# Optimization experiments

Measured on AMD Instinct MI355X. Metric: run time of the kernel, lower is better.

The kernel has to match this reference:

```python
import jax, jax.numpy as jnp
from jax import lax
import numpy as np

B, N, K = 8, 4096, 64          # clouds, points per cloud, max neighbors
N1, N2 = N // 2, N // 8        # fps ratio 0.5, then 0.25
R1, R2 = 0.2, 0.4              # ball-query radii


def setup_inputs() -> dict:
    key = jax.random.key(0)
    ks = jax.random.split(key, 7)
    def w(k, i, o):
        return jax.random.normal(k, (i, o), jnp.float32) / np.sqrt(i).astype(np.float32)
    return {
        "pos": jax.random.uniform(ks[0], (B, N, 3), jnp.float32),
        "w1a": w(ks[1], 3, 64),    "b1a": jnp.zeros(64, jnp.float32),
        "w1b": w(ks[2], 64, 64),   "b1b": jnp.zeros(64, jnp.float32),
        "w2a": w(ks[3], 67, 128),  "b2a": jnp.zeros(128, jnp.float32),
        "w2b": w(ks[4], 128, 128), "b2b": jnp.zeros(128, jnp.float32),
        "w3a": w(ks[5], 131, 256), "b3a": jnp.zeros(256, jnp.float32),
        "w3b": w(ks[6], 256, 1024),"b3b": jnp.zeros(1024, jnp.float32),
    }


def fps(pos, n_samples):
    # farthest point sampling, deterministic start at index 0. pos: [n, 3]
    d0 = jnp.sum((pos - pos[0]) ** 2, axis=-1)
    def step(mind, _):
        nxt = jnp.argmax(mind)
        d = jnp.sum((pos - pos[nxt]) ** 2, axis=-1)
        return jnp.minimum(mind, d), nxt
    _, idxs = lax.scan(step, d0, None, length=n_samples - 1)
    return jnp.concatenate([jnp.zeros((1,), idxs.dtype), idxs])


def ball_query(centers, pts, r):
    # up to K neighbors within radius r (nearest-first); centers are a subset of pts
    d2 = jnp.sum((centers[:, None, :] - pts[None, :, :]) ** 2, axis=-1)  # [M, n]
    neg = jnp.where(d2 <= r * r, -d2, -jnp.inf)
    vals, nbr = lax.top_k(neg, K)
    return nbr, vals > -jnp.inf  # [M, K] indices, validity mask


def mlp(x, w1, b1, w2, b2, relu_last):
    h = jax.nn.relu(x @ w1 + b1) @ w2 + b2
    return jax.nn.relu(h) if relu_last else h


def masked_max(h, mask):
    # max over neighbor axis; every center has itself as a valid neighbor
    return jnp.max(jnp.where(mask[..., None], h, -jnp.inf), axis=1)


def reference(pos, w1a, b1a, w1b, b1b, w2a, b2a, w2b, b2b, w3a, b3a, w3b, b3b):
    def single(p):  # p: [N, 3]
        # SA1: x is None -> per-edge input is relative position only
        idx1 = fps(p, N1)
        c1 = p[idx1]                                   # [N1, 3]
        nbr1, m1 = ball_query(c1, p, R1)               # [N1, K]
        rel1 = p[nbr1] - c1[:, None, :]                # [N1, K, 3]
        x1 = masked_max(mlp(rel1, w1a, b1a, w1b, b1b, True), m1)   # [N1, 64]
        # SA2: per-edge input is [x_j, pos_j - pos_i]
        idx2 = fps(c1, N2)
        c2 = c1[idx2]                                  # [N2, 3]
        nbr2, m2 = ball_query(c2, c1, R2)              # [N2, K]
        feat2 = jnp.concatenate([x1[nbr2], c1[nbr2] - c2[:, None, :]], axis=-1)  # [N2,K,67]
        x2 = masked_max(mlp(feat2, w2a, b2a, w2b, b2b, True), m2)  # [N2, 128]
        # Global SA: MLP on [x, pos] then global max pool
        g = mlp(jnp.concatenate([x2, c2], axis=-1), w3a, b3a, w3b, b3b, False)   # [N2,1024]
        return jnp.max(g, axis=0)                      # [1024]
    return jax.vmap(single)(pos)                       # [B, 1024]
```

## Files before the change

### kernel.cpp

```cpp
#include <hip/hip_runtime.h>
#include <cstdint>
#include <cstddef>


static constexpr int Bc = 8;
static constexpr int Np = 4096;
static constexpr int Kn = 64;
static constexpr int M1 = 2048;
static constexpr int M2 = 512;
static constexpr int LDX = 132;

#define DEVINL __device__ __forceinline__

DEVINL float d2_exact(float ax, float ay, float az, float bx, float by, float bz) {
    float dx = __fsub_rn(ax, bx);
    float dy = __fsub_rn(ay, by);
    float dz = __fsub_rn(az, bz);
    float xx = __fmul_rn(dx, dx);
    float yy = __fmul_rn(dy, dy);
    float zz = __fmul_rn(dz, dz);
    return __fadd_rn(__fadd_rn(xx, yy), zz);
}

template <int CTRL, int RM, int BM>
DEVINL unsigned long long dpp_max_step(unsigned long long k) {
    unsigned lo = (unsigned)k, hi = (unsigned)(k >> 32);
    unsigned slo = (unsigned)__builtin_amdgcn_update_dpp(0, (int)lo, CTRL, RM, BM, true);
    unsigned shi = (unsigned)__builtin_amdgcn_update_dpp(0, (int)hi, CTRL, RM, BM, true);
    unsigned long long s = ((unsigned long long)shi << 32) | (unsigned long long)slo;
    return s > k ? s : k;
}

DEVINL unsigned long long wave_max_u64_dpp(unsigned long long k) {
    k = dpp_max_step<0x111, 0xf, 0xf>(k);
    k = dpp_max_step<0x112, 0xf, 0xf>(k);
    k = dpp_max_step<0x114, 0xf, 0xf>(k);
    k = dpp_max_step<0x118, 0xf, 0xf>(k);
    k = dpp_max_step<0x142, 0xa, 0xf>(k);
    k = dpp_max_step<0x143, 0xc, 0xf>(k);
    return k;
}

DEVINL unsigned mort3(unsigned v) {
    return (v & 1u) | ((v & 2u) << 2) | ((v & 4u) << 4);
}

DEVINL unsigned cell_of(float x, float y, float z) {
    int ix = (int)(x * 8.0f); ix = ix < 0 ? 0 : (ix > 7 ? 7 : ix);
    int iy = (int)(y * 8.0f); iy = iy < 0 ? 0 : (iy > 7 ? 7 : iy);
    int iz = (int)(z * 8.0f); iz = iz < 0 ? 0 : (iz > 7 ? 7 : iz);
    return mort3((unsigned)ix) | (mort3((unsigned)iy) << 1) | (mort3((unsigned)iz) << 2);
}

DEVINL unsigned* scan512(unsigned* h0, unsigned* h1, int t) {
    unsigned* src = h0; unsigned* dst = h1;
    for (int d = 1; d < 512; d <<= 1) {
        unsigned v = src[t];
        if (t >= d) v += src[t - d];
        dst[t] = v;
        __syncthreads();
        unsigned* tmp = src; src = dst; dst = tmp;
    }
    return src;
}

__global__ __launch_bounds__(512)
void fps2x_kernel(const float* __restrict__ pos, float* __restrict__ c1,
                  float* __restrict__ c2, float* __restrict__ X) {
    constexpr int NT = 512;
    __shared__ float scx[Np], scy[Np], scz[Np];
    __shared__ unsigned spk[Np];
    __shared__ float s2c[M1 * 3];
    __shared__ unsigned h0[512], h1[512];
    __shared__ unsigned long long slots[3];
    const int b = blockIdx.x;
    const int t = threadIdx.x;
    const int lane = t & 63;

    {
        constexpr int PT = Np / NT;
        const float* base = pos + (size_t)b * Np * 3;
        float gx[PT], gy[PT], gz[PT];
        unsigned gc[PT];
        #pragma unroll
        for (int j = 0; j < PT; ++j) {
            int p = j * NT + t;
            gx[j] = base[p * 3 + 0];
            gy[j] = base[p * 3 + 1];
            gz[j] = base[p * 3 + 2];
            gc[j] = cell_of(gx[j], gy[j], gz[j]);
        }
        float x0 = base[0], y0 = base[1], z0 = base[2];
        h0[t] = 0;
        if (t == 0) { slots[0] = 0; slots[1] = 0; slots[2] = 0; }
        __syncthreads();
        #pragma unroll
        for (int j = 0; j < PT; ++j) atomicAdd(&h0[gc[j]], 1u);
        __syncthreads();
        unsigned cnt = h0[t];
        unsigned* inc = scan512(h0, h1, t);
        inc[t] -= cnt;
        __syncthreads();
        #pragma unroll
        for (int j = 0; j < PT; ++j) {
            unsigned p = atomicAdd(&inc[gc[j]], 1u);
            scx[p] = gx[j]; scy[p] = gy[j]; scz[p] = gz[j];
            spk[p] = ((0xFFFu - (unsigned)(j * NT + t)) << 12) | p;
        }
        __syncthreads();

        float px[PT], py[PT], pz[PT], mind[PT];
        unsigned oi[PT];
        #pragma unroll
        for (int j = 0; j < PT; ++j) {
            int p = t * PT + j;
            px[j] = scx[p]; py[j] = scy[p]; pz[j] = scz[p];
            oi[j] = spk[p];
        }
        float lox = px[0], hix = px[0], loy = py[0], hiy = py[0], loz = pz[0], hiz = pz[0];
        #pragma unroll
        for (int j = 1; j < PT; ++j) {
            lox = fminf(lox, px[j]); hix = fmaxf(hix, px[j]);
            loy = fminf(loy, py[j]); hiy = fmaxf(hiy, py[j]);
            loz = fminf(loz, pz[j]); hiz = fmaxf(hiz, pz[j]);
        }

        unsigned long long ck = 0;
        #pragma unroll
        for (int j = 0; j < PT; ++j) {
            float d = d2_exact(px[j], py[j], pz[j], x0, y0, z0);
            mind[j] = d;
            unsigned long long kj =
                ((unsigned long long)__float_as_uint(d) << 24) | (unsigned long long)oi[j];
            if (kj > ck) ck = kj;
        }
        float bmax = __uint_as_float((unsigned)(ck >> 24));
        unsigned long long wkey = wave_max_u64_dpp(ck);
        if (lane == 63) atomicMax(&slots[1], wkey);
        if (t == 0) {
            c1[((size_t)b * M1) * 3 + 0] = x0;
            c1[((size_t)b * M1) * 3 + 1] = y0;
            c1[((size_t)b * M1) * 3 + 2] = z0;
            s2c[0] = x0; s2c[1] = y0; s2c[2] = z0;
        }
        int rd = 1, wr = 2, rs = 0;
        for (int s = 1; s < M1; ++s) {
            __syncthreads();
            unsigned long long km = slots[rd];
            if (t == 0) slots[rs] = 0;
            unsigned spos = (unsigned)km & 0xFFFu;
            float cx = scx[spos], cy = scy[spos], cz = scz[spos];
            if (t == 0) {
                c1[((size_t)b * M1 + s) * 3 + 0] = cx;
                c1[((size_t)b * M1 + s) * 3 + 1] = cy;
                c1[((size_t)b * M1 + s) * 3 + 2] = cz;
                s2c[s * 3 + 0] = cx; s2c[s * 3 + 1] = cy; s2c[s * 3 + 2] = cz;
            }
            float dxv = fmaxf(fmaxf(lox - cx, cx - hix), 0.0f);
            float dyv = fmaxf(fmaxf(loy - cy, cy - hiy), 0.0f);
            float dzv = fmaxf(fmaxf(loz - cz, cz - hiz), 0.0f);
            float L = dxv * dxv + dyv * dyv + dzv * dzv;
            bool fire = (L * 0.999f <= bmax);
            if (fire) {
                unsigned long long nck = 0;
                #pragma unroll
                for (int j = 0; j < PT; ++j) {
                    float d = d2_exact(px[j], py[j], pz[j], cx, cy, cz);
                    float m = fminf(mind[j], d);
                    mind[j] = m;
                    unsigned long long kj =
                        ((unsigned long long)__float_as_uint(m) << 24) | (unsigned long long)oi[j];
                    if (kj > nck) nck = kj;
                }
                ck = nck;
                bmax = __uint_as_float((unsigned)(ck >> 24));
            }
            if (__ballot(fire) != 0ull) wkey = wave_max_u64_dpp(ck);
            if (lane == 63) atomicMax(&slots[wr], wkey);
            int nrd = wr; wr = rs; rs = rd; rd = nrd;
        }
    }
    __syncthreads();

    {
        constexpr int PT = M1 / NT;
        float gx[PT], gy[PT], gz[PT];
        unsigned gc[PT];
        #pragma unroll
        for (int j = 0; j < PT; ++j) {
            int p = j * NT + t;
            gx[j] = s2c[p * 3 + 0];
            gy[j] = s2c[p * 3 + 1];
            gz[j] = s2c[p * 3 + 2];
            gc[j] = cell_of(gx[j], gy[j], gz[j]);
        }
        float x0 = s2c[0], y0 = s2c[1], z0 = s2c[2];
        h0[t] = 0;
        if (t == 0) { slots[0] = 0; slots[1] = 0; slots[2] = 0; }
        __syncthreads();
        #pragma unroll
        for (int j = 0; j < PT; ++j) atomicAdd(&h0[gc[j]], 1u);
        __syncthreads();
        unsigned cnt = h0[t];
        unsigned* inc = scan512(h0, h1, t);
        inc[t] -= cnt;
        __syncthreads();
        #pragma unroll
        for (int j = 0; j < PT; ++j) {
            unsigned p = atomicAdd(&inc[gc[j]], 1u);
            scx[p] = gx[j]; scy[p] = gy[j]; scz[p] = gz[j];
            spk[p] = ((0xFFFu - (unsigned)(j * NT + t)) << 12) | p;
        }
        __syncthreads();

        float px[PT], py[PT], pz[PT], mind[PT];
        unsigned oi[PT];
        #pragma unroll
        for (int j = 0; j < PT; ++j) {
            int p = t * PT + j;
            px[j] = scx[p]; py[j] = scy[p]; pz[j] = scz[p];
            oi[j] = spk[p];
        }
        float lox = px[0], hix = px[0], loy = py[0], hiy = py[0], loz = pz[0], hiz = pz[0];
        #pragma unroll
        for (int j = 1; j < PT; ++j) {
            lox = fminf(lox, px[j]); hix = fmaxf(hix, px[j]);
            loy = fminf(loy, py[j]); hiy = fmaxf(hiy, py[j]);
            loz = fminf(loz, pz[j]); hiz = fmaxf(hiz, pz[j]);
        }

        unsigned long long ck = 0;
        #pragma unroll
        for (int j = 0; j < PT; ++j) {
            float d = d2_exact(px[j], py[j], pz[j], x0, y0, z0);
            mind[j] = d;
            unsigned long long kj =
                ((unsigned long long)__float_as_uint(d) << 24) | (unsigned long long)oi[j];
            if (kj > ck) ck = kj;
        }
        float bmax = __uint_as_float((unsigned)(ck >> 24));
        unsigned long long wkey = wave_max_u64_dpp(ck);
        if (lane == 63) atomicMax(&slots[1], wkey);
        if (t == 0) {
            c2[((size_t)b * M2) * 3 + 0] = x0;
            c2[((size_t)b * M2) * 3 + 1] = y0;
            c2[((size_t)b * M2) * 3 + 2] = z0;
            float* xr = X + (size_t)(b * M2) * LDX;
            xr[128] = x0; xr[129] = y0; xr[130] = z0;
        }
        int rd = 1, wr = 2, rs = 0;
        for (int s = 1; s < M2; ++s) {
            __syncthreads();
            unsigned long long km = slots[rd];
            if (t == 0) slots[rs] = 0;
            unsigned spos = (unsigned)km & 0xFFFu;
            float cx = scx[spos], cy = scy[spos], cz = scz[spos];
            if (t == 0) {
                c2[((size_t)b * M2 + s) * 3 + 0] = cx;
                c2[((size_t)b * M2 + s) * 3 + 1] = cy;
                c2[((size_t)b * M2 + s) * 3 + 2] = cz;
                float* xr = X + (size_t)(b * M2 + s) * LDX;
                xr[128] = cx; xr[129] = cy; xr[130] = cz;
            }
            float dxv = fmaxf(fmaxf(lox - cx, cx - hix), 0.0f);
            float dyv = fmaxf(fmaxf(loy - cy, cy - hiy), 0.0f);
            float dzv = fmaxf(fmaxf(loz - cz, cz - hiz), 0.0f);
            float L = dxv * dxv + dyv * dyv + dzv * dzv;
            bool fire = (L * 0.999f <= bmax);
            if (fire) {
                unsigned long long nck = 0;
                #pragma unroll
                for (int j = 0; j < PT; ++j) {
                    float d = d2_exact(px[j], py[j], pz[j], cx, cy, cz);
                    float m = fminf(mind[j], d);
                    mind[j] = m;
                    unsigned long long kj =
                        ((unsigned long long)__float_as_uint(m) << 24) | (unsigned long long)oi[j];
                    if (kj > nck) nck = kj;
                }
                ck = nck;
                bmax = __uint_as_float((unsigned)(ck >> 24));
            }
            if (__ballot(fire) != 0ull) wkey = wave_max_u64_dpp(ck);
            if (lane == 63) atomicMax(&slots[wr], wkey);
            int nrd = wr; wr = rs; rs = rd; rd = nrd;
        }
    }
}

template <int NPT>
__global__ __launch_bounds__(256)
void bq_kernel(const float* __restrict__ pts, const float* __restrict__ ctr,
               int mshift, float r2, int* __restrict__ nbr) {
    constexpr int CH = NPT / 64;
    constexpr int CAP = 1024;
    __shared__ uint2 cbuf[4][CAP];
    const int lane = threadIdx.x & 63;
    const int wl = threadIdx.x >> 6;
    int w = __builtin_amdgcn_readfirstlane((int)(blockIdx.x * 4 + wl));
    const int b = w >> mshift;
    const float* pb = pts + (size_t)b * NPT * 3;
    const float* cp = ctr + (size_t)w * 3;
    float cx = cp[0], cy = cp[1], cz = cp[2];
    const unsigned r2b = __float_as_uint(r2);

    unsigned ub[CH];
    int cnt = 0;
    #pragma unroll
    for (int j = 0; j < CH; ++j) {
        int p = j * 64 + lane;
        float d = d2_exact(pb[p * 3 + 0], pb[p * 3 + 1], pb[p * 3 + 2], cx, cy, cz);
        ub[j] = __float_as_uint(d);
        cnt += __popcll(__ballot(ub[j] <= r2b));
    }
    int* out = nbr + (size_t)w * Kn;
    const unsigned long long lml = (1ull << lane) - 1ull;

    if (cnt <= Kn) {
        int basep = 0;
        #pragma unroll
        for (int j = 0; j < CH; ++j) {
            bool v = ub[j] <= r2b;
            unsigned long long mk = __ballot(v);
            if (v) out[basep + __popcll(mk & lml)] = j * 64 + lane;
            basep += __popcll(mk);
        }
        if (lane >= cnt) out[lane] = -1;
    } else if (cnt <= CAP) {
        uint2* buf = cbuf[wl];
        int basep = 0;
        #pragma unroll
        for (int j = 0; j < CH; ++j) {
            bool v = ub[j] <= r2b;
            unsigned long long mk = __ballot(v);
            if (v) buf[basep + __popcll(mk & lml)] =
                       make_uint2(ub[j], (unsigned)(j * 64 + lane));
            basep += __popcll(mk);
        }
        const int C2 = (cnt + 63) >> 6;
        unsigned cb[CAP / 64], ci[CAP / 64];
        #pragma unroll
        for (int e = 0; e < CAP / 64; ++e) {
            if (e >= C2) break;
            int p = e * 64 + lane;
            uint2 v = buf[p];
            cb[e] = (p < cnt) ? v.x : 0xFFFFFFFFu;
            ci[e] = v.y;
        }
        unsigned lo = 0, hi = r2b;
        while (lo < hi) {
            unsigned mid = lo + ((hi - lo) >> 1);
            int c = 0;
            #pragma unroll
            for (int e = 0; e < CAP / 64; ++e) {
                if (e >= C2) break;
                c += __popcll(__ballot(cb[e] <= mid));
            }
            if (c >= Kn) hi = mid; else lo = mid + 1;
        }
        const unsigned tt = lo;
        int cntLess = 0;
        #pragma unroll
        for (int e = 0; e < CAP / 64; ++e) {
            if (e >= C2) break;
            cntLess += __popcll(__ballot(cb[e] < tt));
        }
        const int quota = Kn - cntLess;
        int baseLt = 0, eqseen = 0;
        #pragma unroll
        for (int e = 0; e < CAP / 64; ++e) {
            if (e >= C2) break;
            bool lt = cb[e] < tt;
            bool eq = cb[e] == tt;
            unsigned long long mlt = __ballot(lt);
            unsigned long long meq = __ballot(eq);
            if (lt) out[baseLt + __popcll(mlt & lml)] = (int)ci[e];
            if (eq) {
                int rr = eqseen + __popcll(meq & lml);
                if (rr < quota) out[cntLess + rr] = (int)ci[e];
            }
            baseLt += __popcll(mlt);
            eqseen += __popcll(meq);
        }
    } else {
        unsigned lo = 0, hi = r2b;
        while (lo < hi) {
            unsigned mid = lo + ((hi - lo) >> 1);
            int c = 0;
            #pragma unroll
            for (int j = 0; j < CH; ++j) c += __popcll(__ballot(ub[j] <= mid));
            if (c >= Kn) hi = mid; else lo = mid + 1;
        }
        const unsigned tt = lo;
        int cntLess = 0;
        #pragma unroll
        for (int j = 0; j < CH; ++j) cntLess += __popcll(__ballot(ub[j] < tt));
        const int quota = Kn - cntLess;
        int baseLt = 0, eqseen = 0;
        #pragma unroll
        for (int j = 0; j < CH; ++j) {
            bool lt = ub[j] < tt;
            bool eq = ub[j] == tt;
            unsigned long long mlt = __ballot(lt);
            unsigned long long meq = __ballot(eq);
            if (lt) out[baseLt + __popcll(mlt & lml)] = j * 64 + lane;
            if (eq) {
                int rr = eqseen + __popcll(meq & lml);
                if (rr < quota) out[cntLess + rr] = j * 64 + lane;
            }
            baseLt += __popcll(mlt);
            eqseen += __popcll(meq);
        }
    }
}

__global__ __launch_bounds__(256)
void mlp1_kernel(const float* __restrict__ pos, const float* __restrict__ c1,
                 const int* __restrict__ nbr, const float* __restrict__ w1aT,
                 const float* __restrict__ w1bT, const float* __restrict__ b1b,
                 float* __restrict__ x1) {
    const int lane = threadIdx.x & 63;
    int w = __builtin_amdgcn_readfirstlane((int)(blockIdx.x * 4 + (threadIdx.x >> 6)));
    const int b = w >> 11;
    const int ii = nbr[(size_t)w * Kn + lane];
    const bool valid = ii >= 0;
    const int i2 = valid ? ii : 0;
    const float* pp = pos + ((size_t)b * Np + i2) * 3;
    const float* cc = c1 + (size_t)w * 3;
    float rx = pp[0] - cc[0], ry = pp[1] - cc[1], rz = pp[2] - cc[2];
    float h1[64];
    #pragma unroll
    for (int h = 0; h < 64; ++h) {
        float4 wv = ((const float4*)w1aT)[h];
        float a = fmaf(rx, wv.x, fmaf(ry, wv.y, fmaf(rz, wv.z, wv.w)));
        h1[h] = fmaxf(a, 0.0f);
    }
    float* orow = x1 + (size_t)w * 64;
    for (int c4 = 0; c4 < 16; ++c4) {
        float v4[4];
        #pragma unroll
        for (int cq = 0; cq < 4; ++cq) {
            int c = c4 * 4 + cq;
            float acc = b1b[c];
            const float4* wr = (const float4*)(w1bT + (size_t)c * 64);
            #pragma unroll
            for (int q = 0; q < 16; ++q) {
                float4 wv = wr[q];
                acc = fmaf(h1[4 * q + 0], wv.x, acc);
                acc = fmaf(h1[4 * q + 1], wv.y, acc);
                acc = fmaf(h1[4 * q + 2], wv.z, acc);
                acc = fmaf(h1[4 * q + 3], wv.w, acc);
            }
            float v = fmaxf(acc, 0.0f);
            v = valid ? v : -__builtin_inff();
            #pragma unroll
            for (int o = 32; o > 0; o >>= 1) v = fmaxf(v, __shfl_xor(v, o, 64));
            v4[cq] = v;
        }
        if (lane == 0)
            ((float4*)orow)[c4] = make_float4(v4[0], v4[1], v4[2], v4[3]);
    }
}

__global__ __launch_bounds__(256)
void mlp2_kernel(const float* __restrict__ x1, const float* __restrict__ c1,
                 const float* __restrict__ c2, const int* __restrict__ nbr2,
                 const float* __restrict__ w2aT, const float* __restrict__ w2bT,
                 const float* __restrict__ b2b, float* __restrict__ X) {
    const int lane = threadIdx.x & 63;
    int w = __builtin_amdgcn_readfirstlane((int)(blockIdx.x * 4 + (threadIdx.x >> 6)));
    const int b = w >> 9;
    const int ii = nbr2[(size_t)w * Kn + lane];
    const bool valid = ii >= 0;
    const int i2 = valid ? ii : 0;

    float x[68];
    const float4* xr = (const float4*)(x1 + ((size_t)b * M1 + i2) * 64);
    #pragma unroll
    for (int q = 0; q < 16; ++q) {
        float4 v = xr[q];
        x[4 * q + 0] = v.x; x[4 * q + 1] = v.y;
        x[4 * q + 2] = v.z; x[4 * q + 3] = v.w;
    }
    const float* cc = c2 + (size_t)w * 3;
    const float* cp = c1 + ((size_t)b * M1 + i2) * 3;
    x[64] = cp[0] - cc[0];
    x[65] = cp[1] - cc[1];
    x[66] = cp[2] - cc[2];
    x[67] = 0.0f;

    float h1[128];
    #pragma unroll
    for (int h = 0; h < 128; ++h) {
        const float4* r4 = (const float4*)(w2aT + (size_t)h * 80);
        float acc = 0.0f;
        #pragma unroll
        for (int q = 0; q < 16; ++q) {
            float4 wv = r4[q];
            acc = fmaf(x[4 * q + 0], wv.x, acc);
            acc = fmaf(x[4 * q + 1], wv.y, acc);
            acc = fmaf(x[4 * q + 2], wv.z, acc);
            acc = fmaf(x[4 * q + 3], wv.w, acc);
        }
        float4 tl = r4[16];
        acc = fmaf(x[64], tl.x, acc);
        acc = fmaf(x[65], tl.y, acc);
        acc = fmaf(x[66], tl.z, acc);
        acc += tl.w;
        h1[h] = fmaxf(acc, 0.0f);
    }
    float* orow = X + (size_t)w * LDX;
    for (int c4 = 0; c4 < 32; ++c4) {
        float v4[4];
        #pragma unroll
        for (int cq = 0; cq < 4; ++cq) {
            int c = c4 * 4 + cq;
            float acc = b2b[c];
            const float4* wr = (const float4*)(w2bT + (size_t)c * 128);
            #pragma unroll
            for (int q = 0; q < 32; ++q) {
                float4 wv = wr[q];
                acc = fmaf(h1[4 * q + 0], wv.x, acc);
                acc = fmaf(h1[4 * q + 1], wv.y, acc);
                acc = fmaf(h1[4 * q + 2], wv.z, acc);
                acc = fmaf(h1[4 * q + 3], wv.w, acc);
            }
            float v = fmaxf(acc, 0.0f);
            v = valid ? v : -__builtin_inff();
            #pragma unroll
            for (int o = 32; o > 0; o >>= 1) v = fmaxf(v, __shfl_xor(v, o, 64));
            v4[cq] = v;
        }
        if (lane == 0) {
            orow[c4 * 4 + 0] = v4[0]; orow[c4 * 4 + 1] = v4[1];
            orow[c4 * 4 + 2] = v4[2]; orow[c4 * 4 + 3] = v4[3];
        }
    }
}

__global__ __launch_bounds__(256)
void gemm1_kernel(const float* __restrict__ X, const float* __restrict__ w3a,
                  const float* __restrict__ b3a, float* __restrict__ H) {
    const int r = blockIdx.x;
    const int c = threadIdx.x;
    const float* xr = X + (size_t)r * LDX;
    float acc = b3a[c];
    for (int i = 0; i < 131; ++i)
        acc = fmaf(xr[i], w3a[(size_t)i * 256 + c], acc);
    H[(size_t)r * 256 + c] = fmaxf(acc, 0.0f);
}

__global__ __launch_bounds__(256)
void gemm2_kernel(const float* __restrict__ H, const float* __restrict__ w3b,
                  float* __restrict__ part) {
    __shared__ float As[32][33];
    __shared__ float Bs[32][64];
    __shared__ float red[8][64];
    const int bidx = blockIdx.x;
    const int nt = bidx & 15;
    const int mt = (bidx >> 4) & 15;
    const int b = bidx >> 8;
    const int row0 = b * M2 + mt * 32;
    const int col0 = nt * 64;
    const int t = threadIdx.x;
    const int rg = t >> 5, cg = t & 31;

    float acc[4][2] = {{0.f, 0.f}, {0.f, 0.f}, {0.f, 0.f}, {0.f, 0.f}};
    for (int k0 = 0; k0 < 256; k0 += 32) {
        #pragma unroll
        for (int q = 0; q < 4; ++q) {
            int id = t + q * 256;
            As[id >> 5][id & 31] = H[(size_t)(row0 + (id >> 5)) * 256 + k0 + (id & 31)];
        }
        #pragma unroll
        for (int q = 0; q < 8; ++q) {
            int id = t + q * 256;
            Bs[id >> 6][id & 63] = w3b[(size_t)(k0 + (id >> 6)) * 1024 + col0 + (id & 63)];
        }
        __syncthreads();
        #pragma unroll
        for (int kk = 0; kk < 32; ++kk) {
            float b0 = Bs[kk][cg * 2 + 0];
            float b1 = Bs[kk][cg * 2 + 1];
            #pragma unroll
            for (int j = 0; j < 4; ++j) {
                float a = As[rg * 4 + j][kk];
                acc[j][0] = fmaf(a, b0, acc[j][0]);
                acc[j][1] = fmaf(a, b1, acc[j][1]);
            }
        }
        __syncthreads();
    }
    float m0 = fmaxf(fmaxf(acc[0][0], acc[1][0]), fmaxf(acc[2][0], acc[3][0]));
    float m1 = fmaxf(fmaxf(acc[0][1], acc[1][1]), fmaxf(acc[2][1], acc[3][1]));
    red[rg][cg * 2 + 0] = m0;
    red[rg][cg * 2 + 1] = m1;
    __syncthreads();
    if (t < 64) {
        float v = red[0][t];
        #pragma unroll
        for (int q = 1; q < 8; ++q) v = fmaxf(v, red[q][t]);
        part[((size_t)b * 16 + mt) * 1024 + col0 + t] = v;
    }
}

__global__ __launch_bounds__(256)
void rmax_kernel(const float* __restrict__ part, const float* __restrict__ b3b,
                 float* __restrict__ out) {
    int i = blockIdx.x * 256 + threadIdx.x;
    int b = i >> 10, c = i & 1023;
    float v = -__builtin_inff();
    #pragma unroll
    for (int tt = 0; tt < 16; ++tt)
        v = fmaxf(v, part[((size_t)b * 16 + tt) * 1024 + c]);
    out[i] = v + b3b[c];
}

__global__ __launch_bounds__(256)
void prep_kernel(const float* __restrict__ w1a, const float* __restrict__ b1a,
                 const float* __restrict__ w1b, const float* __restrict__ w2a,
                 const float* __restrict__ b2a, const float* __restrict__ w2b,
                 float* __restrict__ w1aT, float* __restrict__ w1bT,
                 float* __restrict__ w2aT, float* __restrict__ w2bT) {
    int i = blockIdx.x * 256 + threadIdx.x;
    if (i < 64 * 4) {
        int h = i >> 2, d = i & 3;
        w1aT[i] = (d < 3) ? w1a[d * 64 + h] : b1a[h];
    }
    if (i < 64 * 64) {
        int c = i >> 6, h = i & 63;
        w1bT[i] = w1b[h * 64 + c];
    }
    if (i < 128 * 80) {
        int h = i / 80, d = i - h * 80;
        w2aT[i] = (d < 67) ? w2a[d * 128 + h] : ((d == 67) ? b2a[h] : 0.0f);
    }
    {
        int c = i >> 7, h = i & 127;
        w2bT[i] = w2b[h * 128 + c];
    }
}

extern "C" void kernel_launch(void* const* d_in, const int* in_sizes, int n_in,
                              void* d_out, int out_size, void* d_ws, size_t ws_size,
                              hipStream_t stream) {
    const float* pos = (const float*)d_in[0];
    const float* w1a = (const float*)d_in[1];
    const float* b1a = (const float*)d_in[2];
    const float* w1b = (const float*)d_in[3];
    const float* b1b = (const float*)d_in[4];
    const float* w2a = (const float*)d_in[5];
    const float* b2a = (const float*)d_in[6];
    const float* w2b = (const float*)d_in[7];
    const float* b2b = (const float*)d_in[8];
    const float* w3a = (const float*)d_in[9];
    const float* b3a = (const float*)d_in[10];
    const float* w3b = (const float*)d_in[11];
    const float* b3b = (const float*)d_in[12];
    float* out = (float*)d_out;

    char* ws = (char*)d_ws;
    size_t off = 0;
    auto alloc = [&](size_t bytes) -> char* {
        char* p = ws + off;
        off += (bytes + 255) & ~(size_t)255;
        return p;
    };
    float* c1   = (float*)alloc(sizeof(float) * Bc * M1 * 3);
    float* c2   = (float*)alloc(sizeof(float) * Bc * M2 * 3);
    int*   nbr1 = (int*)alloc(sizeof(int) * Bc * M1 * Kn);
    int*   nbr2 = (int*)alloc(sizeof(int) * Bc * M2 * Kn);
    float* x1   = (float*)alloc(sizeof(float) * Bc * M1 * 64);
    float* X    = (float*)alloc(sizeof(float) * Bc * M2 * LDX);
    float* H    = (float*)alloc(sizeof(float) * Bc * M2 * 256);
    float* part = (float*)alloc(sizeof(float) * Bc * 16 * 1024);
    float* w1aT = (float*)alloc(sizeof(float) * 64 * 4);
    float* w1bT = (float*)alloc(sizeof(float) * 64 * 64);
    float* w2aT = (float*)alloc(sizeof(float) * 128 * 80);
    float* w2bT = (float*)alloc(sizeof(float) * 128 * 128);

    prep_kernel<<<dim3(64), dim3(256), 0, stream>>>(w1a, b1a, w1b, w2a, b2a, w2b,
                                                    w1aT, w1bT, w2aT, w2bT);
    fps2x_kernel<<<dim3(Bc), dim3(512), 0, stream>>>(pos, c1, c2, X);
    bq_kernel<Np><<<dim3(Bc * M1 / 4), dim3(256), 0, stream>>>(
        pos, c1, 11, (float)(0.2 * 0.2), nbr1);
    mlp1_kernel<<<dim3(Bc * M1 / 4), dim3(256), 0, stream>>>(
        pos, c1, nbr1, w1aT, w1bT, b1b, x1);
    bq_kernel<M1><<<dim3(Bc * M2 / 4), dim3(256), 0, stream>>>(
        c1, c2, 9, (float)(0.4 * 0.4), nbr2);
    mlp2_kernel<<<dim3(Bc * M2 / 4), dim3(256), 0, stream>>>(
        x1, c1, c2, nbr2, w2aT, w2bT, b2b, X);
    gemm1_kernel<<<dim3(Bc * M2), dim3(256), 0, stream>>>(X, w3a, b3a, H);
    gemm2_kernel<<<dim3(Bc * 16 * 16), dim3(256), 0, stream>>>(H, w3b, part);
    rmax_kernel<<<dim3(32), dim3(256), 0, stream>>>(part, b3b, out);
}
```

Before: 2.501 ms.

## Replace per-step block barrier in FPS with tagged per-wave LDS flag polling

The farthest-point-sampling loops used a __syncthreads plus a shared atomicMax slot ring every iteration to agree on the next sample. Each wave now writes its tagged max key into a double-buffered per-wave slot. Every wave spins on volatile LDS reads until all eight slots carry the current step tag, then reduces them locally. This drops the block-wide barrier and the LDS atomics, but relies on volatile LDS ordering and busy-wait polling between waves, which carries correctness and forward-progress risk if waves are not co-scheduled or memory ordering is weak.

New measurement: 3.435 ms. 1.37x slower.

```diff
diff --git a/kernel.cpp b/kernel.cpp
--- a/kernel.cpp
+++ b/kernel.cpp
@@ -68,14 +68,17 @@
 void fps2x_kernel(const float* __restrict__ pos, float* __restrict__ c1,
                   float* __restrict__ c2, float* __restrict__ X) {
     constexpr int NT = 512;
+    constexpr unsigned long long TM = 0xFF00000000000000ull;
+    constexpr unsigned long long KM = 0x00FFFFFFFFFFFFFFull;
     __shared__ float scx[Np], scy[Np], scz[Np];
     __shared__ unsigned spk[Np];
     __shared__ float s2c[M1 * 3];
     __shared__ unsigned h0[512], h1[512];
-    __shared__ unsigned long long slots[3];
+    __shared__ alignas(16) unsigned long long pbuf[2][8];
     const int b = blockIdx.x;
     const int t = threadIdx.x;
     const int lane = t & 63;
+    const int wid = t >> 6;
 
     {
         constexpr int PT = Np / NT;
@@ -92,7 +95,7 @@
         }
         float x0 = base[0], y0 = base[1], z0 = base[2];
         h0[t] = 0;
-        if (t == 0) { slots[0] = 0; slots[1] = 0; slots[2] = 0; }
+        if (t < 16) pbuf[t >> 3][t & 7] = 0;
         __syncthreads();
         #pragma unroll
         for (int j = 0; j < PT; ++j) atomicAdd(&h0[gc[j]], 1u);
@@ -136,18 +139,34 @@
         }
         float bmax = __uint_as_float((unsigned)(ck >> 24));
         unsigned long long wkey = wave_max_u64_dpp(ck);
-        if (lane == 63) atomicMax(&slots[1], wkey);
+        if (lane == 63) pbuf[1][wid] = (1ull << 56) | wkey;
         if (t == 0) {
             c1[((size_t)b * M1) * 3 + 0] = x0;
             c1[((size_t)b * M1) * 3 + 1] = y0;
             c1[((size_t)b * M1) * 3 + 2] = z0;
             s2c[0] = x0; s2c[1] = y0; s2c[2] = z0;
         }
-        int rd = 1, wr = 2, rs = 0;
         for (int s = 1; s < M1; ++s) {
-            __syncthreads();
-            unsigned long long km = slots[rd];
-            if (t == 0) slots[rs] = 0;
+            const unsigned long long tg = (unsigned long long)(s & 0xFF) << 56;
+            volatile unsigned long long* vb = &pbuf[s & 1][0];
+            unsigned long long v0, v1, v2, v3, v4, v5, v6, v7;
+            for (;;) {
+                v0 = vb[0]; v1 = vb[1]; v2 = vb[2]; v3 = vb[3];
+                v4 = vb[4]; v5 = vb[5]; v6 = vb[6]; v7 = vb[7];
+                if (((v0 & TM) == tg) & ((v1 & TM) == tg) &
+                    ((v2 & TM) == tg) & ((v3 & TM) == tg) &
+                    ((v4 & TM) == tg) & ((v5 & TM) == tg) &
+                    ((v6 & TM) == tg) & ((v7 & TM) == tg)) break;
+            }
+            v0 &= KM; v1 &= KM; v2 &= KM; v3 &= KM;
+            v4 &= KM; v5 &= KM; v6 &= KM; v7 &= KM;
+            unsigned long long a0 = v0 > v1 ? v0 : v1;
+            unsigned long long a1 = v2 > v3 ? v2 : v3;
+            unsigned long long a2 = v4 > v5 ? v4 : v5;
+            unsigned long long a3 = v6 > v7 ? v6 : v7;
+            unsigned long long ka = a0 > a1 ? a0 : a1;
+            unsigned long long kb = a2 > a3 ? a2 : a3;
+            unsigned long long km = ka > kb ? ka : kb;
             unsigned spos = (unsigned)km & 0xFFFu;
             float cx = scx[spos], cy = scy[spos], cz = scz[spos];
             if (t == 0) {
@@ -176,8 +195,9 @@
                 bmax = __uint_as_float((unsigned)(ck >> 24));
             }
             if (__ballot(fire) != 0ull) wkey = wave_max_u64_dpp(ck);
-            if (lane == 63) atomicMax(&slots[wr], wkey);
-            int nrd = wr; wr = rs; rs = rd; rd = nrd;
+            if (lane == 63)
+                pbuf[(s + 1) & 1][wid] =
+                    ((unsigned long long)((s + 1) & 0xFF) << 56) | wkey;
         }
     }
     __syncthreads();
@@ -196,7 +216,7 @@
         }
         float x0 = s2c[0], y0 = s2c[1], z0 = s2c[2];
         h0[t] = 0;
-        if (t == 0) { slots[0] = 0; slots[1] = 0; slots[2] = 0; }
+        if (t < 16) pbuf[t >> 3][t & 7] = 0;
         __syncthreads();
         #pragma unroll
         for (int j = 0; j < PT; ++j) atomicAdd(&h0[gc[j]], 1u);
@@ -240,7 +260,7 @@
         }
         float bmax = __uint_as_float((unsigned)(ck >> 24));
         unsigned long long wkey = wave_max_u64_dpp(ck);
-        if (lane == 63) atomicMax(&slots[1], wkey);
+        if (lane == 63) pbuf[1][wid] = (1ull << 56) | wkey;
         if (t == 0) {
             c2[((size_t)b * M2) * 3 + 0] = x0;
             c2[((size_t)b * M2) * 3 + 1] = y0;
@@ -248,11 +268,27 @@
             float* xr = X + (size_t)(b * M2) * LDX;
             xr[128] = x0; xr[129] = y0; xr[130] = z0;
         }
-        int rd = 1, wr = 2, rs = 0;
         for (int s = 1; s < M2; ++s) {
-            __syncthreads();
-            unsigned long long km = slots[rd];
-            if (t == 0) slots[rs] = 0;
+            const unsigned long long tg = (unsigned long long)(s & 0xFF) << 56;
+            volatile unsigned long long* vb = &pbuf[s & 1][0];
+            unsigned long long v0, v1, v2, v3, v4, v5, v6, v7;
+            for (;;) {
+                v0 = vb[0]; v1 = vb[1]; v2 = vb[2]; v3 = vb[3];
+                v4 = vb[4]; v5 = vb[5]; v6 = vb[6]; v7 = vb[7];
+                if (((v0 & TM) == tg) & ((v1 & TM) == tg) &
+                    ((v2 & TM) == tg) & ((v3 & TM) == tg) &
+                    ((v4 & TM) == tg) & ((v5 & TM) == tg) &
+                    ((v6 & TM) == tg) & ((v7 & TM) == tg)) break;
+            }
+            v0 &= KM; v1 &= KM; v2 &= KM; v3 &= KM;
+            v4 &= KM; v5 &= KM; v6 &= KM; v7 &= KM;
+            unsigned long long a0 = v0 > v1 ? v0 : v1;
+            unsigned long long a1 = v2 > v3 ? v2 : v3;
+            unsigned long long a2 = v4 > v5 ? v4 : v5;
+            unsigned long long a3 = v6 > v7 ? v6 : v7;
+            unsigned long long ka = a0 > a1 ? a0 : a1;
+            unsigned long long kb = a2 > a3 ? a2 : a3;
+            unsigned long long km = ka > kb ? ka : kb;
             unsigned spos = (unsigned)km & 0xFFFu;
             float cx = scx[spos], cy = scy[spos], cz = scz[spos];
             if (t == 0) {
@@ -282,8 +318,9 @@
                 bmax = __uint_as_float((unsigned)(ck >> 24));
             }
             if (__ballot(fire) != 0ull) wkey = wave_max_u64_dpp(ck);
-            if (lane == 63) atomicMax(&slots[wr], wkey);
-            int nrd = wr; wr = rs; rs = rd; rd = nrd;
+            if (lane == 63)
+                pbuf[(s + 1) & 1][wid] =
+                    ((unsigned long long)((s + 1) & 0xFF) << 56) | wkey;
         }
     }
 }
```
